# Kernel optimization log

Measured on AMD Instinct MI355X. Metric: run time of the kernel, lower is better.

Reference implementation:

```python
import jax, jax.numpy as jnp
import numpy as np

B, N, L, D = 4096, 11, 12, 256
ZDIM = 32
LINE_DIM = 64
PAST_DIM = 6 * D - (2 * D + LINE_DIM)  # 960


def _pos_enc(length, d):
    # PositionalAgentEncoding.build_pos_enc
    pos = jnp.arange(length, dtype=jnp.float32)[:, None]
    div = jnp.exp(jnp.arange(0, d, 2, dtype=jnp.float32) * (-np.log(10000.0) / d))
    pe = jnp.zeros((length, d), dtype=jnp.float32)
    pe = pe.at[:, 0::2].set(jnp.sin(pos * div))
    pe = pe.at[:, 1::2].set(jnp.cos(pos * div))
    return pe


def setup_inputs() -> dict:
    key = jax.random.key(0)
    ks = jax.random.split(key, 16)
    s = 0.02
    return {
        "inputs": jax.random.normal(ks[0], (B * N, L, 4), jnp.float32),
        "past_feature": jax.random.normal(ks[1], (B * N, PAST_DIM), jnp.float32),
        "W_in": jax.random.normal(ks[2], (4, D), jnp.float32) * s,
        "b_in": jnp.zeros((D,), jnp.float32),
        "W_pos": jax.random.normal(ks[3], (2 * D, D), jnp.float32) * s,
        "b_pos": jnp.zeros((D,), jnp.float32),
        "W_fc2": jax.random.normal(ks[4], (L * D, D), jnp.float32) * s,
        "b_fc2": jnp.zeros((D,), jnp.float32),
        "W_fc3": jax.random.normal(ks[5], (D + N, D), jnp.float32) * s,
        "b_fc3": jnp.zeros((D,), jnp.float32),
        "W_msg": jax.random.normal(ks[6], (2 * D, D), jnp.float32) * s,
        "b_msg": jnp.zeros((D,), jnp.float32),
        "W_hyp": jax.random.normal(ks[7], (2 * D, D), jnp.float32) * s,
        "b_hyp": jnp.zeros((D,), jnp.float32),
        "W_line": jax.random.normal(ks[8], (D, LINE_DIM), jnp.float32) * s,
        "W_out": jax.random.normal(ks[9], (6 * D, 128), jnp.float32) * s,
        "b_out": jnp.zeros((128,), jnp.float32),
        "W_qz": jax.random.normal(ks[10], (128, 2 * ZDIM), jnp.float32) * s,
        "b_qz": jnp.zeros((2 * ZDIM,), jnp.float32),
        "batch_size": B,
        "agent_num": N,
    }


def reference(inputs, past_feature, W_in, b_in, W_pos, b_pos, W_fc2, b_fc2,
              W_fc3, b_fc3, W_msg, b_msg, W_hyp, b_hyp, W_line,
              W_out, b_out, W_qz, b_qz, batch_size, agent_num):
    BN, length, _ = inputs.shape
    d = W_in.shape[1]
    bsz, n = batch_size, agent_num
    # input_fc + positional encoding (concat=True, dropout=eval identity)
    tf = inputs @ W_in + b_in                                   # [BN, L, D]
    pe = jnp.broadcast_to(_pos_enc(length, d), (BN, length, d))
    tf = jnp.concatenate([tf, pe], axis=-1) @ W_pos + b_pos     # [BN, L, D]
    # input_fc2 over flattened time, then category concat + input_fc3
    ftraj = tf.reshape(bsz, n, length * d) @ W_fc2 + b_fc2      # [B, N, D]
    cat = jnp.broadcast_to(jnp.eye(n, dtype=ftraj.dtype), (bsz, n, n))
    ftraj = jnp.concatenate([ftraj, cat], axis=-1) @ W_fc3 + b_fc3
    # cosine correlation + per-scene adaptive threshold
    q = ftraj / jnp.linalg.norm(ftraj, axis=2, keepdims=True)
    corr = jnp.einsum('bnd,bmd->bnm', q, q)                     # [B, N, N]
    a = corr.min(axis=(1, 2))
    thr = jnp.where(a < 0.4, 0.4,
                    jnp.where((a > 0.4) & (a < 0.6), a + 0.1, a + 0.03))
    corr = jnp.where(corr < thr[:, None, None], 0.0, corr)
    # ordinary MS_HGNN surrogate: one dense message-passing round
    attn = jax.nn.softmax(jnp.einsum('bnd,bmd->bnm', ftraj, ftraj)
                          / jnp.sqrt(jnp.asarray(d, ftraj.dtype)), axis=-1)
    agg = jnp.einsum('bnm,bmd->bnd', attn, ftraj)
    ftraj_inter = jax.nn.relu(jnp.concatenate([ftraj, agg], -1) @ W_msg + b_msg)
    # hyper/clique surrogate: binarized thresholded corr as incidence, degree-normalized
    A = (corr > 0).astype(ftraj.dtype)
    A = A / jnp.maximum(A.sum(-1, keepdims=True), 1.0)
    hag = jnp.einsum('bnm,bmd->bnd', A, ftraj)
    hyp = jax.nn.relu(jnp.concatenate([ftraj, hag], -1) @ W_hyp + b_hyp)
    feat_bs = hyp @ W_line                                      # [B, N, 64]
    final = jnp.concatenate([ftraj, ftraj_inter, feat_bs], -1).reshape(bsz * n, -1)
    h = jnp.concatenate([past_feature, final], axis=-1)         # [BN, 6D]
    h = jax.nn.relu(h @ W_out + b_out)
    return h @ W_qz + b_qz                                      # [BN, 2*zdim]
```

## Files before the change

### kernel.cpp

```cpp
#include <hip/hip_runtime.h>
#include <hip/hip_bf16.h>

#define BB 4096
#define NNA 11
#define BN (BB*NNA)

#define OFF_WEFF   0
#define OFF_BIASL  1024
#define OFF_WBIG   4096
#define OFF_WALL   16640
#define OFF_WG1F   31744
#define OFF_BIASG1 87040
#define OFF_WG2    99712
#define OFF_WQT    198656
#define OFF_P2T    202752
#define OFF_P3T    205824
#define OFF_MIX    296320
#define OFF_INTER  1287552

typedef short bh8 __attribute__((ext_vector_type(8)));
typedef float fx4 __attribute__((ext_vector_type(4)));

__device__ __forceinline__ short f2bs(float v) { __hip_bfloat16 h = __float2bfloat16(v); return *(short*)&h; }


__global__ __launch_bounds__(256) void k_p1(const float* W_in, const float* b_in,
                                            const float* W_pos, const float* b_pos,
                                            float* ws) {
  __shared__ float A[16*512];
  __shared__ float red[4*16*64];
  int t = threadIdx.x, cb = blockIdx.x;
  int ks = t >> 6, c = t & 63, col = cb*64 + c;
  float coef = -logf(10000.f) / 256.f;
  for (int i = t; i < 16*512; i += 256) {
    int row = i >> 9, kk = i & 511;
    float v;
    if (row < 4) v = (kk < 256) ? W_in[row*256 + kk] : 0.f;
    else if (kk < 256) v = b_in[kk];
    else {
      int ii = (kk - 256) >> 1;
      float dv = expf(coef * (float)(2*ii));
      float ang = (float)(row - 4) * dv;
      v = (kk & 1) ? cosf(ang) : sinf(ang);
    }
    A[i] = v;
  }
  __syncthreads();
  float acc[16];
  #pragma unroll
  for (int r = 0; r < 16; ++r) acc[r] = 0.f;
  #pragma unroll 4
  for (int j = 0; j < 128; ++j) {
    int jj = ks*128 + j;
    float b = W_pos[(size_t)jj*256 + col];
    #pragma unroll
    for (int r = 0; r < 16; ++r) acc[r] += A[r*512 + jj] * b;
  }
  #pragma unroll
  for (int r = 0; r < 16; ++r) red[(ks*16 + r)*64 + c] = acc[r];
  __syncthreads();
  for (int i = t; i < 16*64; i += 256) {
    int row = i >> 6, cc = i & 63;
    float s = red[row*64+cc] + red[(16+row)*64+cc] + red[(32+row)*64+cc] + red[(48+row)*64+cc];
    int gcol = cb*64 + cc;
    if (row < 4) ws[OFF_WEFF + row*256 + gcol] = s;
    else         ws[OFF_BIASL + (row-4)*256 + gcol] = s + b_pos[gcol];
  }
}

__global__ __launch_bounds__(256) void k_p2(const float* W_fc2, float* ws) {
  __shared__ float A[5*256];
  __shared__ float red[4*5*64];
  int t = threadIdx.x, cb = blockIdx.x, l = blockIdx.y;
  int ks = t >> 6, c = t & 63, col = cb*64 + c;
  for (int i = t; i < 5*256; i += 256) {
    int row = i >> 8, kk = i & 255;
    A[i] = (row < 4) ? ws[OFF_WEFF + row*256 + kk] : ws[OFF_BIASL + l*256 + kk];
  }
  __syncthreads();
  float acc[5] = {0.f, 0.f, 0.f, 0.f, 0.f};
  #pragma unroll 4
  for (int j = 0; j < 64; ++j) {
    int jj = ks*64 + j;
    float b = W_fc2[(size_t)(l*256 + jj)*256 + col];
    #pragma unroll
    for (int r = 0; r < 5; ++r) acc[r] += A[r*256 + jj] * b;
  }
  #pragma unroll
  for (int r = 0; r < 5; ++r) red[(ks*5 + r)*64 + c] = acc[r];
  __syncthreads();
  for (int i = t; i < 5*64; i += 256) {
    int row = i / 64, cc = i % 64;
    float s = red[row*64+cc] + red[(5+row)*64+cc] + red[(10+row)*64+cc] + red[(15+row)*64+cc];
    int gcol = cb*64 + cc;
    if (row < 4) ws[OFF_WBIG + (l*4 + row)*256 + gcol] = s;
    else         ws[OFF_P2T + l*256 + gcol] = s;
  }
}

__global__ __launch_bounds__(256) void k_p3(const float* W_fc3, const float* b_fc2, float* ws) {
  __shared__ float A[7*256];
  __shared__ float red[4*7*64];
  int t = threadIdx.x, cb = blockIdx.x, rg = blockIdx.y;
  int ks = t >> 6, c = t & 63, col = cb*64 + c;
  for (int i = t; i < 7*256; i += 256) {
    int row = i >> 8, kk = i & 255, gr = rg*7 + row;
    float v;
    if (gr < 48) v = ws[OFF_WBIG + gr*256 + kk];
    else {
      v = b_fc2[kk];
      #pragma unroll
      for (int l = 0; l < 12; ++l) v += ws[OFF_P2T + l*256 + kk];
    }
    A[i] = v;
  }
  __syncthreads();
  float acc[7] = {0.f,0.f,0.f,0.f,0.f,0.f,0.f};
  #pragma unroll 4
  for (int j = 0; j < 64; ++j) {
    int jj = ks*64 + j;
    float b = W_fc3[(size_t)jj*256 + col];
    #pragma unroll
    for (int r = 0; r < 7; ++r) acc[r] += A[r*256 + jj] * b;
  }
  #pragma unroll
  for (int r = 0; r < 7; ++r) red[(ks*7 + r)*64 + c] = acc[r];
  __syncthreads();
  for (int i = t; i < 7*64; i += 256) {
    int row = i / 64, cc = i % 64, gr = rg*7 + row;
    float s = red[row*64+cc] + red[(7+row)*64+cc] + red[(14+row)*64+cc] + red[(21+row)*64+cc];
    int gcol = cb*64 + cc;
    if (gr < 48)       ws[OFF_WALL + gr*256 + gcol] = s;
    else if (gr == 48) ws[OFF_P3T + gcol] = s;
  }
}

__device__ __forceinline__ float wg1_elem(int j, int col, const float* W_msg,
                                          const float* W_hyp, const float* W_out) {
  if (col < 256)       return W_msg[j*256 + col];
  else if (col < 512)  return W_msg[(256+j)*256 + (col-256)];
  else if (col < 768)  return W_hyp[j*256 + (col-512)];
  else if (col < 1024) return W_hyp[(256+j)*256 + (col-768)];
  else                 return W_out[(960+j)*128 + (col-1024)];
}

__global__ __launch_bounds__(256) void k_p4(const float* W_msg, const float* b_msg,
                                            const float* W_hyp, const float* b_hyp,
                                            const float* W_out, const float* W_fc3,
                                            const float* b_fc3, float* ws) {
  __shared__ float A[8*256];
  __shared__ float red[4*8*64];
  int t = threadIdx.x, cb = blockIdx.x, rg = blockIdx.y;
  int ks = t >> 6, c = t & 63, col = cb*64 + c;
  for (int i = t; i < 8*256; i += 256) {
    int row = i >> 8, kk = i & 255, gr = rg*8 + row;
    float v;
    if (gr < 48)      v = ws[OFF_WALL + gr*256 + kk];
    else if (gr < 59) v = ws[OFF_P3T + kk] + b_fc3[kk] + W_fc3[(size_t)(256 + gr - 48)*256 + kk];
    else              v = 0.f;
    A[i] = v;
  }
  __syncthreads();
  float acc[8];
  #pragma unroll
  for (int r = 0; r < 8; ++r) acc[r] = 0.f;
  #pragma unroll 4
  for (int j = 0; j < 64; ++j) {
    int jj = ks*64 + j;
    float b = wg1_elem(jj, col, W_msg, W_hyp, W_out);
    #pragma unroll
    for (int r = 0; r < 8; ++r) acc[r] += A[r*256 + jj] * b;
  }
  #pragma unroll
  for (int r = 0; r < 8; ++r) red[(ks*8 + r)*64 + c] = acc[r];
  __syncthreads();
  for (int i = t; i < 8*64; i += 256) {
    int row = i >> 6, cc = i & 63, gr = rg*8 + row;
    float s = red[row*64+cc] + red[(8+row)*64+cc] + red[(16+row)*64+cc] + red[(24+row)*64+cc];
    int gcol = cb*64 + cc;
    if (gr < 48) {
      ws[OFF_WG1F + gr*1152 + gcol] = s;
    } else if (gr < 59) {
      if (gcol < 256) s += b_msg[gcol];
      else if (gcol >= 512 && gcol < 768) s += b_hyp[gcol-512];
      ws[OFF_BIASG1 + (gr-48)*1152 + gcol] = s;
    }
  }
}

__global__ __launch_bounds__(128) void k_p5(const float* W_line, const float* W_out,
                                            const float* W_qz, float* ws) {
  int t = threadIdx.x;
  if (blockIdx.x >= 1536) {
    int i = (blockIdx.x - 1536)*128 + t;
    int n = i >> 7, k = i & 127;
    short* WQs = (short*)(ws + OFF_WQT);
    WQs[n*128 + k] = f2bs(W_qz[k*64 + n]);
    return;
  }
  int c = t, r = blockIdx.x;
  float v;
  if (r < 960)       v = W_out[r*128 + c];
  else if (r < 1216) v = W_out[(r+256)*128 + c];
  else if (r < 1472) {
    int dd = r - 1216;
    float s = 0.f;
    for (int j = 0; j < 64; ++j)
      s += W_line[dd*64 + j] * W_out[(1472+j)*128 + c];
    v = s;
  } else if (r < 1520) {
    v = ws[OFF_WG1F + (r-1472)*1152 + 1024 + c];
  } else v = 0.f;
  short* WTs = (short*)(ws + OFF_WG2);
  WTs[(size_t)c*1536 + r] = f2bs(v);
}

__global__ __launch_bounds__(256) void k_front(const float* __restrict__ inputs,
                                               const float* __restrict__ W_fc3,
                                               const float* __restrict__ b_fc3,
                                               float* __restrict__ ws) {
  __shared__ float F[44*260];
  __shared__ float C[4*121];
  int t = threadIdx.x;
  int R0 = blockIdx.x * 44;
  {
    int d = t;
    float acc[44];
    float base = ws[OFF_P3T + d] + b_fc3[d];
    #pragma unroll
    for (int r = 0; r < 44; ++r) acc[r] = base + W_fc3[(size_t)(256 + (r % 11))*256 + d];
    for (int k = 0; k < 48; ++k) {
      float w = ws[OFF_WALL + k*256 + d];
      #pragma unroll
      for (int r = 0; r < 44; ++r)
        acc[r] += inputs[(size_t)(R0 + r)*48 + k] * w;
    }
    #pragma unroll
    for (int r = 0; r < 44; ++r) F[r*260 + d] = acc[r];
  }
  __syncthreads();
  int w = t >> 6, lane = t & 63;
  {
    const float4* F4 = (const float4*)F;
    for (int p = lane; p < 66; p += 64) {
      int n = 0, pp = p;
      while (pp >= 11 - n) { pp -= 11 - n; ++n; }
      int m = n + pp;
      int ra = (w*11 + n) * 65, rb2 = (w*11 + m) * 65;
      float s = 0.f;
      #pragma unroll 4
      for (int j = 0; j < 64; ++j) {
        float4 a = F4[ra + j], b = F4[rb2 + j];
        s += a.x*b.x + a.y*b.y + a.z*b.z + a.w*b.w;
      }
      C[w*121 + n*11 + m] = s;
      C[w*121 + m*11 + n] = s;
    }
  }
  __syncthreads();
  {
    float* Cw = C + w*121;
    float rn[11];
    #pragma unroll
    for (int n = 0; n < 11; ++n) rn[n] = 1.f / sqrtf(Cw[n*11+n]);
    float a = 1e30f;
    for (int n = 0; n < 11; ++n)
      for (int m = 0; m < 11; ++m)
        a = fminf(a, Cw[n*11+m] * rn[n] * rn[m]);
    float thr = (a < 0.4f) ? 0.4f : (((a > 0.4f) && (a < 0.6f)) ? a + 0.1f : a + 0.03f);
    int scene = blockIdx.x*4 + w;
    float* mixb = ws + OFF_MIX + (size_t)scene*242;
    if (lane < 11) {
      int n = lane;
      float mx = -1e30f;
      #pragma unroll
      for (int m = 0; m < 11; ++m) mx = fmaxf(mx, Cw[n*11+m]);
      mx *= (1.f/16.f);
      float e[11], ssum = 0.f;
      #pragma unroll
      for (int m = 0; m < 11; ++m) { e[m] = expf(Cw[n*11+m]*(1.f/16.f) - mx); ssum += e[m]; }
      float inv = 1.f / ssum;
      #pragma unroll
      for (int m = 0; m < 11; ++m) mixb[n*11+m] = e[m]*inv;
      float keep[11], cnt = 0.f;
      #pragma unroll
      for (int m = 0; m < 11; ++m) {
        float q = Cw[n*11+m] * rn[n] * rn[m];
        keep[m] = (q >= thr) ? 1.f : 0.f; cnt += keep[m];
      }
      float sc = 1.f / fmaxf(cnt, 1.f);
      #pragma unroll
      for (int m = 0; m < 11; ++m) mixb[121 + n*11 + m] = keep[m]*sc;
    }
  }
}

__global__ __launch_bounds__(256) void k_mix(const float* __restrict__ inputs,
                                             const float* __restrict__ ws,
                                             __hip_bfloat16* __restrict__ outI,
                                             __hip_bfloat16* __restrict__ outH) {
  int t = threadIdx.x;
  int s0 = blockIdx.x * 2;
  int R0 = s0 * 11;
  int gy = blockIdx.y;
  __hip_bfloat16* dst = gy ? outH : outI;
  int gc = gy*512 + t;
  float accT[22], accB[22];
  #pragma unroll
  for (int r = 0; r < 22; ++r) {
    accT[r] = ws[OFF_BIASG1 + (r % 11)*1152 + gc];
    accB[r] = ws[OFF_BIASG1 + (r % 11)*1152 + gc + 256];
  }
  for (int k = 0; k < 48; ++k) {
    float wt = ws[OFF_WG1F + k*1152 + gc];
    float wb = ws[OFF_WG1F + k*1152 + gc + 256];
    #pragma unroll
    for (int r = 0; r < 22; ++r) {
      float xv = inputs[(size_t)(R0 + r)*48 + k];
      accT[r] += xv * wt;
      accB[r] += xv * wb;
    }
  }
  #pragma unroll
  for (int s = 0; s < 2; ++s)
    #pragma unroll
    for (int n = 0; n < 11; ++n) {
      float v = accT[s*11+n];
      #pragma unroll
      for (int m = 0; m < 11; ++m)
        v += ws[OFF_MIX + (size_t)(s0+s)*242 + gy*121 + n*11 + m] * accB[s*11+m];
      v = fmaxf(v, 0.f);
      dst[(size_t)(R0 + s*11 + n)*256 + t] = __float2bfloat16(v);
    }
}

#define A_OFF 0
#define BT_OFF 4608
#define HS_OFF 0
#define WQ_OFF 8704
__global__ __launch_bounds__(256) void k_g2(const float* past, const float* inputs,
                                            const float* b_out, const float* b_qz,
                                            const __hip_bfloat16* interI, const __hip_bfloat16* hypI,
                                            float* ws, float* out) {
  __shared__ short LDS[18432];
  int t = threadIdx.x;
  int R0 = blockIdx.x * 64;
  int w = t >> 6, lane = t & 63, quad = lane >> 4, l16 = lane & 15;
  const short* WTs = (const short*)(ws + OFF_WG2);
  const short* WQs = (const short*)(ws + OFF_WQT);
  const short* intS = (const short*)interI;
  const short* hypS = (const short*)hypI;

  fx4 acc[4][2];
  #pragma unroll
  for (int mt = 0; mt < 4; ++mt)
    #pragma unroll
    for (int reg = 0; reg < 4; ++reg) {
      int nidx = (R0 + mt*16 + quad*4 + reg) % 11;
      #pragma unroll
      for (int nt = 0; nt < 2; ++nt) {
        int col = w*32 + nt*16 + l16;
        acc[mt][nt][reg] = b_out[col] + ws[OFF_BIASG1 + nidx*1152 + 1024 + col];
      }
    }

  int ar = t >> 2, akq = (t & 3) * 16;
  int bn = t >> 1, bkh = (t & 1) * 32;
  for (int ch = 0; ch < 24; ++ch) {
    __syncthreads();
    {
      short tmp[16];
      if (ch < 15) {
        const float4* sp = (const float4*)(past + (size_t)(R0+ar)*960 + ch*64 + akq);
        #pragma unroll
        for (int q = 0; q < 4; ++q) {
          float4 v = sp[q];
          tmp[4*q+0]=f2bs(v.x); tmp[4*q+1]=f2bs(v.y); tmp[4*q+2]=f2bs(v.z); tmp[4*q+3]=f2bs(v.w);
        }
        *(bh8*)&LDS[A_OFF + ar*72 + akq]     = *(bh8*)&tmp[0];
        *(bh8*)&LDS[A_OFF + ar*72 + akq + 8] = *(bh8*)&tmp[8];
      } else if (ch < 23) {
        const short* s = ((ch < 19) ? intS : hypS) + (size_t)(R0+ar)*256 + ((ch < 19) ? (ch-15) : (ch-19))*64 + akq;
        *(bh8*)&LDS[A_OFF + ar*72 + akq]     = *(const bh8*)&s[0];
        *(bh8*)&LDS[A_OFF + ar*72 + akq + 8] = *(const bh8*)&s[8];
      } else {
        if (akq < 48) {
          const float4* sp = (const float4*)(inputs + (size_t)(R0+ar)*48 + akq);
          #pragma unroll
          for (int q = 0; q < 4; ++q) {
            float4 v = sp[q];
            tmp[4*q+0]=f2bs(v.x); tmp[4*q+1]=f2bs(v.y); tmp[4*q+2]=f2bs(v.z); tmp[4*q+3]=f2bs(v.w);
          }
        } else {
          #pragma unroll
          for (int q = 0; q < 16; ++q) tmp[q] = 0;
        }
        *(bh8*)&LDS[A_OFF + ar*72 + akq]     = *(bh8*)&tmp[0];
        *(bh8*)&LDS[A_OFF + ar*72 + akq + 8] = *(bh8*)&tmp[8];
      }
    }
    {
      const short* s = WTs + (size_t)bn*1536 + ch*64 + bkh;
      #pragma unroll
      for (int q = 0; q < 4; ++q)
        *(bh8*)&LDS[BT_OFF + bn*72 + bkh + q*8] = *(const bh8*)&s[q*8];
    }
    __syncthreads();
    #pragma unroll
    for (int ks = 0; ks < 2; ++ks) {
      int kk = ks*32 + quad*8;
      bh8 a[4], b[2];
      #pragma unroll
      for (int mt = 0; mt < 4; ++mt) a[mt] = *(const bh8*)&LDS[A_OFF + (mt*16 + l16)*72 + kk];
      #pragma unroll
      for (int nt = 0; nt < 2; ++nt) b[nt] = *(const bh8*)&LDS[BT_OFF + (w*32 + nt*16 + l16)*72 + kk];
      #pragma unroll
      for (int mt = 0; mt < 4; ++mt)
        #pragma unroll
        for (int nt = 0; nt < 2; ++nt)
          acc[mt][nt] = __builtin_amdgcn_mfma_f32_16x16x32_bf16(a[mt], b[nt], acc[mt][nt], 0, 0, 0);
    }
  }
  __syncthreads();
  #pragma unroll
  for (int mt = 0; mt < 4; ++mt)
    #pragma unroll
    for (int nt = 0; nt < 2; ++nt)
      #pragma unroll
      for (int reg = 0; reg < 4; ++reg)
        LDS[HS_OFF + (mt*16 + quad*4 + reg)*136 + w*32 + nt*16 + l16] = f2bs(fmaxf(acc[mt][nt][reg], 0.f));
  {
    int n = t >> 2, kh = (t & 3) * 32;
    const short* s = WQs + n*128 + kh;
    #pragma unroll
    for (int q = 0; q < 4; ++q)
      *(bh8*)&LDS[WQ_OFF + n*136 + kh + q*8] = *(const bh8*)&s[q*8];
  }
  __syncthreads();
  fx4 acc2[4];
  {
    float bq = b_qz[w*16 + l16];
    #pragma unroll
    for (int mt = 0; mt < 4; ++mt) { acc2[mt][0]=bq; acc2[mt][1]=bq; acc2[mt][2]=bq; acc2[mt][3]=bq; }
  }
  #pragma unroll
  for (int ks = 0; ks < 4; ++ks) {
    int kk = ks*32 + quad*8;
    bh8 bb = *(const bh8*)&LDS[WQ_OFF + (w*16 + l16)*136 + kk];
    #pragma unroll
    for (int mt = 0; mt < 4; ++mt) {
      bh8 aa = *(const bh8*)&LDS[HS_OFF + (mt*16 + l16)*136 + kk];
      acc2[mt] = __builtin_amdgcn_mfma_f32_16x16x32_bf16(aa, bb, acc2[mt], 0, 0, 0);
    }
  }
  #pragma unroll
  for (int mt = 0; mt < 4; ++mt)
    #pragma unroll
    for (int reg = 0; reg < 4; ++reg)
      out[(size_t)(R0 + mt*16 + quad*4 + reg)*64 + w*16 + l16] = acc2[mt][reg];
}

extern "C" void kernel_launch(void* const* d_in, const int* in_sizes, int n_in,
                              void* d_out, int out_size, void* d_ws, size_t ws_size,
                              hipStream_t stream) {
  const float* inputs = (const float*)d_in[0];
  const float* past   = (const float*)d_in[1];
  const float* W_in   = (const float*)d_in[2];
  const float* b_in   = (const float*)d_in[3];
  const float* W_pos  = (const float*)d_in[4];
  const float* b_pos  = (const float*)d_in[5];
  const float* W_fc2  = (const float*)d_in[6];
  const float* b_fc2  = (const float*)d_in[7];
  const float* W_fc3  = (const float*)d_in[8];
  const float* b_fc3  = (const float*)d_in[9];
  const float* W_msg  = (const float*)d_in[10];
  const float* b_msg  = (const float*)d_in[11];
  const float* W_hyp  = (const float*)d_in[12];
  const float* b_hyp  = (const float*)d_in[13];
  const float* W_line = (const float*)d_in[14];
  const float* W_out  = (const float*)d_in[15];
  const float* b_out  = (const float*)d_in[16];
  const float* W_qz   = (const float*)d_in[17];
  const float* b_qz   = (const float*)d_in[18];
  float* ws = (float*)d_ws;
  __hip_bfloat16* interI = (__hip_bfloat16*)(ws + OFF_INTER);
  __hip_bfloat16* hypI   = interI + (size_t)BN*256;
  float* outp   = (float*)d_out;

  hipLaunchKernelGGL(k_p1,  dim3(4),      dim3(256), 0, stream, W_in, b_in, W_pos, b_pos, ws);
  hipLaunchKernelGGL(k_p2,  dim3(4, 12),  dim3(256), 0, stream, W_fc2, ws);
  hipLaunchKernelGGL(k_p3,  dim3(4, 7),   dim3(256), 0, stream, W_fc3, b_fc2, ws);
  hipLaunchKernelGGL(k_p4,  dim3(18, 8),  dim3(256), 0, stream, W_msg, b_msg, W_hyp, b_hyp, W_out, W_fc3, b_fc3, ws);
  hipLaunchKernelGGL(k_p5,  dim3(1600),   dim3(128), 0, stream, W_line, W_out, W_qz, ws);
  hipLaunchKernelGGL(k_front, dim3(1024), dim3(256), 0, stream, inputs, W_fc3, b_fc3, ws);
  hipLaunchKernelGGL(k_mix, dim3(2048, 2), dim3(256), 0, stream, inputs, ws, interI, hypI);
  hipLaunchKernelGGL(k_g2,  dim3(704),    dim3(256), 0, stream, past, inputs, b_out, b_qz,
                     interI, hypI, ws, outp);
}
```

Measured before the change: 570.9 us.

## Stage inputs transposed in LDS and merge k_mix y-grid into one block

k_front and k_mix now stage their block's input rows into shared memory transposed, so the inner k-loop reads float4 vectors from LDS instead of issuing scalar global loads per row. k_mix also drops the two-way blockIdx.y split: each block computes both the inter and hyper outputs, which reuses the staged inputs and halves the input reloads. The per-sample mixing matrices are preloaded into LDS. In exchange k_mix holds 96 accumulators per thread under launch_bounds(256,2), so register pressure rises and occupancy may drop, and there is half as many blocks.

```diff
diff --git a/kernel.cpp b/kernel.cpp
--- a/kernel.cpp
+++ b/kernel.cpp
@@ -215,14 +215,18 @@
   WTs[(size_t)c*1536 + r] = f2bs(v);
 }
 
-__global__ __launch_bounds__(256) void k_front(const float* __restrict__ inputs,
-                                               const float* __restrict__ W_fc3,
-                                               const float* __restrict__ b_fc3,
-                                               float* __restrict__ ws) {
+__global__ __launch_bounds__(256) void k_front(const float* inputs, const float* W_fc3,
+                                               const float* b_fc3, float* ws) {
+  __shared__ float XT[48*44];
   __shared__ float F[44*260];
   __shared__ float C[4*121];
   int t = threadIdx.x;
   int R0 = blockIdx.x * 44;
+  for (int i = t; i < 44*48; i += 256) {
+    int r = i / 48, k = i - r*48;
+    XT[k*44 + r] = inputs[(size_t)(R0+r)*48 + k];
+  }
+  __syncthreads();
   {
     int d = t;
     float acc[44];
@@ -232,8 +236,11 @@
     for (int k = 0; k < 48; ++k) {
       float w = ws[OFF_WALL + k*256 + d];
       #pragma unroll
-      for (int r = 0; r < 44; ++r)
-        acc[r] += inputs[(size_t)(R0 + r)*48 + k] * w;
+      for (int j = 0; j < 11; ++j) {
+        float4 xv = *(const float4*)&XT[k*44 + 4*j];
+        acc[4*j+0] += xv.x*w; acc[4*j+1] += xv.y*w;
+        acc[4*j+2] += xv.z*w; acc[4*j+3] += xv.w*w;
+      }
     }
     #pragma unroll
     for (int r = 0; r < 44; ++r) F[r*260 + d] = acc[r];
@@ -295,42 +302,62 @@
   }
 }
 
-__global__ __launch_bounds__(256) void k_mix(const float* __restrict__ inputs,
-                                             const float* __restrict__ ws,
-                                             __hip_bfloat16* __restrict__ outI,
-                                             __hip_bfloat16* __restrict__ outH) {
+__global__ __launch_bounds__(256, 2) void k_mix(const float* inputs, float* ws,
+                                             __hip_bfloat16* outI, __hip_bfloat16* outH) {
+  __shared__ float XT[48*24];
+  __shared__ float MW[4*121];
   int t = threadIdx.x;
   int s0 = blockIdx.x * 2;
   int R0 = s0 * 11;
-  int gy = blockIdx.y;
-  __hip_bfloat16* dst = gy ? outH : outI;
-  int gc = gy*512 + t;
-  float accT[22], accB[22];
-  #pragma unroll
-  for (int r = 0; r < 22; ++r) {
-    accT[r] = ws[OFF_BIASG1 + (r % 11)*1152 + gc];
-    accB[r] = ws[OFF_BIASG1 + (r % 11)*1152 + gc + 256];
+  for (int i = t; i < 22*48; i += 256) {
+    int r = i / 48, k = i - r*48;
+    XT[k*24 + r] = inputs[(size_t)(R0+r)*48 + k];
+  }
+  for (int i = t; i < 96; i += 256) { int k = i >> 1, r = 22 + (i & 1); XT[k*24+r] = 0.f; }
+  for (int i = t; i < 484; i += 256) {
+    int gy = i / 242, j = i - gy*242;
+    int s = j / 121, jj = j - s*121;
+    MW[(gy*2 + s)*121 + jj] = ws[OFF_MIX + (size_t)(s0+s)*242 + gy*121 + jj];
+  }
+  __syncthreads();
+  float aT0[24], aB0[24], aT1[24], aB1[24];
+  #pragma unroll
+  for (int r = 0; r < 24; ++r) {
+    if (r < 22) {
+      int nb = OFF_BIASG1 + (r % 11)*1152 + t;
+      aT0[r] = ws[nb];
+      aB0[r] = ws[nb + 256];
+      aT1[r] = ws[nb + 512];
+      aB1[r] = ws[nb + 768];
+    } else { aT0[r]=0.f; aB0[r]=0.f; aT1[r]=0.f; aB1[r]=0.f; }
   }
   for (int k = 0; k < 48; ++k) {
-    float wt = ws[OFF_WG1F + k*1152 + gc];
-    float wb = ws[OFF_WG1F + k*1152 + gc + 256];
-    #pragma unroll
-    for (int r = 0; r < 22; ++r) {
-      float xv = inputs[(size_t)(R0 + r)*48 + k];
-      accT[r] += xv * wt;
-      accB[r] += xv * wb;
+    float wt0 = ws[OFF_WG1F + k*1152 + t];
+    float wb0 = ws[OFF_WG1F + k*1152 + t + 256];
+    float wt1 = ws[OFF_WG1F + k*1152 + t + 512];
+    float wb1 = ws[OFF_WG1F + k*1152 + t + 768];
+    #pragma unroll
+    for (int j = 0; j < 6; ++j) {
+      float4 xv = *(const float4*)&XT[k*24 + 4*j];
+      aT0[4*j+0] += xv.x*wt0; aT0[4*j+1] += xv.y*wt0; aT0[4*j+2] += xv.z*wt0; aT0[4*j+3] += xv.w*wt0;
+      aB0[4*j+0] += xv.x*wb0; aB0[4*j+1] += xv.y*wb0; aB0[4*j+2] += xv.z*wb0; aB0[4*j+3] += xv.w*wb0;
+      aT1[4*j+0] += xv.x*wt1; aT1[4*j+1] += xv.y*wt1; aT1[4*j+2] += xv.z*wt1; aT1[4*j+3] += xv.w*wt1;
+      aB1[4*j+0] += xv.x*wb1; aB1[4*j+1] += xv.y*wb1; aB1[4*j+2] += xv.z*wb1; aB1[4*j+3] += xv.w*wb1;
     }
   }
   #pragma unroll
   for (int s = 0; s < 2; ++s)
     #pragma unroll
     for (int n = 0; n < 11; ++n) {
-      float v = accT[s*11+n];
-      #pragma unroll
-      for (int m = 0; m < 11; ++m)
-        v += ws[OFF_MIX + (size_t)(s0+s)*242 + gy*121 + n*11 + m] * accB[s*11+m];
-      v = fmaxf(v, 0.f);
-      dst[(size_t)(R0 + s*11 + n)*256 + t] = __float2bfloat16(v);
+      float v0 = aT0[s*11+n];
+      float v1 = aT1[s*11+n];
+      #pragma unroll
+      for (int m = 0; m < 11; ++m) {
+        v0 += MW[s*121 + n*11 + m]       * aB0[s*11+m];
+        v1 += MW[(2+s)*121 + n*11 + m]   * aB1[s*11+m];
+      }
+      outI[(size_t)(R0 + s*11 + n)*256 + t] = __float2bfloat16(fmaxf(v0, 0.f));
+      outH[(size_t)(R0 + s*11 + n)*256 + t] = __float2bfloat16(fmaxf(v1, 0.f));
     }
 }
 
@@ -493,7 +520,7 @@
   hipLaunchKernelGGL(k_p4,  dim3(18, 8),  dim3(256), 0, stream, W_msg, b_msg, W_hyp, b_hyp, W_out, W_fc3, b_fc3, ws);
   hipLaunchKernelGGL(k_p5,  dim3(1600),   dim3(128), 0, stream, W_line, W_out, W_qz, ws);
   hipLaunchKernelGGL(k_front, dim3(1024), dim3(256), 0, stream, inputs, W_fc3, b_fc3, ws);
-  hipLaunchKernelGGL(k_mix, dim3(2048, 2), dim3(256), 0, stream, inputs, ws, interI, hypI);
+  hipLaunchKernelGGL(k_mix, dim3(2048),   dim3(256), 0, stream, inputs, ws, interI, hypI);
   hipLaunchKernelGGL(k_g2,  dim3(704),    dim3(256), 0, stream, past, inputs, b_out, b_qz,
                      interI, hypI, ws, outp);
 }
```

Result: faster. 496.0 us (-13.1%).
